# Performance work log

Hardware: AMD Instinct MI355X
Metric: run time of the kernel (lower is better)

## Reference

```python
import jax, jax.numpy as jnp
import numpy as np
from jax import lax

B = 16384
N_NUM = 32
N_CAT = 16
D = 256
D_HID = 512
N_LAYERS = 8
VOCAB = 100001  # total_cats + 1
OUT_DIM = 2
TOT_FEAT = N_NUM + N_CAT
EPS = 1e-5


def _layernorm(x, g, b):
    mu = jnp.mean(x, axis=-1, keepdims=True)
    var = jnp.mean(jnp.square(x - mu), axis=-1, keepdims=True)
    return (x - mu) * lax.rsqrt(var + EPS) * g + b


def setup_inputs() -> dict:
    key = jax.random.key(0)
    ks = jax.random.split(key, 16)
    s = 0.02
    return {
        "x_numerical": jax.random.normal(ks[0], (B, N_NUM, 1), dtype=jnp.float32),
        "x_categorical_idx": jax.random.randint(ks[1], (B, N_CAT), 0, VOCAB - 1, dtype=jnp.int32),
        # per-feature Linear(1, D): weight [N_NUM, D], bias [N_NUM, D]
        "w_num": jax.random.normal(ks[2], (N_NUM, D), dtype=jnp.float32) * s,
        "b_num": jnp.zeros((N_NUM, D), dtype=jnp.float32),
        "cat_embed": jax.random.normal(ks[3], (VOCAB, D), dtype=jnp.float32) * s,
        "W_first": jax.random.normal(ks[4], (TOT_FEAT * D, D), dtype=jnp.float32) * s,
        "b_first": jnp.zeros((D,), dtype=jnp.float32),
        # stacked block params, leading dim = N_LAYERS
        "ln_g": jnp.ones((N_LAYERS, D), dtype=jnp.float32),
        "ln_b": jnp.zeros((N_LAYERS, D), dtype=jnp.float32),
        "W1s": jax.random.normal(ks[5], (N_LAYERS, D, D_HID), dtype=jnp.float32) * s,
        "b1s": jnp.zeros((N_LAYERS, D_HID), dtype=jnp.float32),
        "W2s": jax.random.normal(ks[6], (N_LAYERS, D_HID, D), dtype=jnp.float32) * s,
        "b2s": jnp.zeros((N_LAYERS, D), dtype=jnp.float32),
        "g_f": jnp.ones((D,), dtype=jnp.float32),
        "beta_f": jnp.zeros((D,), dtype=jnp.float32),
        "W_head": jax.random.normal(ks[7], (D, OUT_DIM), dtype=jnp.float32) * s,
        "b_head": jnp.zeros((OUT_DIM,), dtype=jnp.float32),
    }


def reference(x_numerical, x_categorical_idx, w_num, b_num, cat_embed,
              W_first, b_first, ln_g, ln_b, W1s, b1s, W2s, b2s,
              g_f, beta_f, W_head, b_head):
    # numerical embeddings: per-feature Linear(1, D), vectorized over features
    x_val = x_numerical[:, :, 0:1]                       # [B, N_NUM, 1]
    x_n_emb = x_val * w_num[None] + b_num[None]          # [B, N_NUM, D]
    x_c_emb = cat_embed[x_categorical_idx]               # [B, N_CAT, D]
    x = jnp.concatenate([x_n_emb, x_c_emb], axis=1)      # [B, TOT_FEAT, D]
    x = x.reshape(x.shape[0], -1)                        # [B, TOT_FEAT*D]
    x = x @ W_first + b_first                            # [B, D]

    def block(h, params):
        g, bn, W1, b1, W2, b2 = params
        out = _layernorm(h, g, bn)
        out = jax.nn.relu(out @ W1 + b1)                 # dropout = identity (eval)
        out = out @ W2 + b2
        return h + out, None

    x, _ = lax.scan(block, x, (ln_g, ln_b, W1s, b1s, W2s, b2s))
    x = _layernorm(x, g_f, beta_f)
    logits = x @ W_head + b_head                         # [B, OUT_DIM]
    return logits
```

## Files before the change

kernel.cpp:

```cpp
#include <hip/hip_runtime.h>

typedef unsigned short u16;
typedef unsigned int u32;
typedef __attribute__((ext_vector_type(8))) short bf16x8;
typedef __attribute__((ext_vector_type(4))) float f32x4;

#define LDK 72

__device__ __forceinline__ u16 f2bf(float f) {
    u32 u = __float_as_uint(f);
    u += 0x7fffu + ((u >> 16) & 1u);
    return (u16)(u >> 16);
}

__device__ __forceinline__ f32x4 mfma16(bf16x8 a, bf16x8 b, f32x4 c) {
    return __builtin_amdgcn_mfma_f32_16x16x32_bf16(a, b, c, 0, 0, 0);
}


__global__ __launch_bounds__(256) void prep_u_kernel(
    const float* __restrict__ w_num, const float* __restrict__ b_num,
    const float* __restrict__ W_first, float* __restrict__ U, float* __restrict__ P)
{
    __shared__ float wrow[256];
    __shared__ float brow[256];
    int j = threadIdx.x, f = blockIdx.x;
    wrow[j] = w_num[f * 256 + j];
    brow[j] = b_num[f * 256 + j];
    __syncthreads();
    float au = 0.f, ap = 0.f;
#pragma unroll 8
    for (int k = 0; k < 256; k++) {
        float w = W_first[(size_t)((f << 8) + k) * 256 + j];
        au = fmaf(wrow[k], w, au);
        ap = fmaf(brow[k], w, ap);
    }
    U[f * 256 + j] = au;
    P[f * 256 + j] = ap;
}

__global__ __launch_bounds__(256) void prep_c0_kernel(
    const float* __restrict__ b_first, const float* __restrict__ P, float* __restrict__ c0)
{
    int j = threadIdx.x;
    float a = b_first[j];
#pragma unroll 8
    for (int f = 0; f < 32; f++) a += P[f * 256 + j];
    c0[j] = a;
}

__global__ __launch_bounds__(256) void transpose_kernel(
    const float* __restrict__ in, u16* __restrict__ out,
    int R, int C, int ldo, int k_off, size_t in_stride, size_t out_stride)
{
    __shared__ float t[64][65];
    in  += (size_t)blockIdx.z * in_stride;
    out += (size_t)blockIdx.z * out_stride;
    const int tid = threadIdx.x;
    const int r0 = blockIdx.x * 64, c0 = blockIdx.y * 64;
#pragma unroll
    for (int i = 0; i < 16; i++) {
        int e = tid + i * 256;
        int r = e >> 6, c = e & 63;
        float v = (r0 + r < R) ? in[(size_t)(r0 + r) * C + c0 + c] : 0.f;
        t[c][r] = v;
    }
    __syncthreads();
#pragma unroll
    for (int i = 0; i < 2; i++) {
        int e = tid + i * 256;
        int c = e >> 3, r8 = (e & 7) * 8;
        u16 tmp[8];
#pragma unroll
        for (int x = 0; x < 8; x++) tmp[x] = f2bf(t[c][r8 + x]);
        *(bf16x8*)&out[(size_t)(c0 + c) * ldo + k_off + r0 + r8] = *(bf16x8*)tmp;
    }
}

#define FBM 64

#define GATHER(KQ, G0, G1)                                                    \
    {                                                                         \
        int chunk = tid;                                                      \
        int r = chunk >> 4, c4 = chunk & 15;                                  \
        int k = (KQ) + c4 * 4;                                                \
        int rowi = (k < 4096) ? sidx[r * 16 + ((k >> 8) & 15)] : 0;           \
        G0 = *(const float4*)&cemb[(size_t)rowi * 256 + (k & 255)];           \
        if (k >= 4096) {                                                      \
            if (k < 4128) {                                                   \
                int c = r * 32 + (k - 4096);                                  \
                G0.x = sx[c]; G0.y = sx[c + 1];                               \
                G0.z = sx[c + 2]; G0.w = sx[c + 3];                           \
            } else G0 = make_float4(0.f, 0.f, 0.f, 0.f);                      \
        }                                                                     \
        chunk = tid + 512;                                                    \
        r = chunk >> 4; c4 = chunk & 15;                                      \
        k = (KQ) + c4 * 4;                                                    \
        rowi = (k < 4096) ? sidx[r * 16 + ((k >> 8) & 15)] : 0;               \
        G1 = *(const float4*)&cemb[(size_t)rowi * 256 + (k & 255)];           \
        if (k >= 4096) {                                                      \
            if (k < 4128) {                                                   \
                int c = r * 32 + (k - 4096);                                  \
                G1.x = sx[c]; G1.y = sx[c + 1];                               \
                G1.z = sx[c + 2]; G1.w = sx[c + 3];                           \
            } else G1 = make_float4(0.f, 0.f, 0.f, 0.f);                      \
        }                                                                     \
    }

#define WRITE_A(BUF, G0, G1)                                                  \
    {                                                                         \
        int chunk = tid;                                                      \
        int r = chunk >> 4, c4 = chunk & 15;                                  \
        ushort4 o;                                                            \
        o.x = f2bf(G0.x); o.y = f2bf(G0.y); o.z = f2bf(G0.z); o.w = f2bf(G0.w); \
        *(ushort4*)&Ab[BUF][r * LDK + c4 * 4] = o;                            \
        chunk = tid + 512;                                                    \
        r = chunk >> 4; c4 = chunk & 15;                                      \
        o.x = f2bf(G1.x); o.y = f2bf(G1.y); o.z = f2bf(G1.z); o.w = f2bf(G1.w); \
        *(ushort4*)&Ab[BUF][r * LDK + c4 * 4] = o;                            \
    }

#define DMA_B(BUF, KQ)                                                        \
    _Pragma("unroll")                                                         \
    for (int it = 0; it < 4; it++) {                                          \
        int chunk = it * 512 + tid;                                           \
        int r = chunk >> 3;                                                   \
        int c8 = (chunk & 7) ^ (r & 7);                                       \
        const u16* src = &BT[(size_t)r * 4160 + (KQ) + c8 * 8];               \
        __builtin_amdgcn_global_load_lds(                                     \
            (const __attribute__((address_space(1))) void*)src,               \
            (__attribute__((address_space(3))) void*)&Bb[BUF][(it * 512 + wv * 64) * 8], \
            16, 0, 0);                                                        \
    }

#define COMPUTE(CUR)                                                          \
    _Pragma("unroll")                                                         \
    for (int kk = 0; kk < 64; kk += 32) {                                     \
        bf16x8 af[2], bfr[4];                                                 \
        _Pragma("unroll")                                                     \
        for (int i = 0; i < 2; i++)                                           \
            af[i] = *(const bf16x8*)&Ab[CUR][(wm * 32 + i * 16 + l16) * LDK + kk + quad * 8]; \
        _Pragma("unroll")                                                     \
        for (int j = 0; j < 4; j++) {                                         \
            int row = wn * 64 + j * 16 + l16;                                 \
            int c8L = quad + (kk >> 3);                                       \
            bfr[j] = *(const bf16x8*)&Bb[CUR][row * 64 + ((c8L ^ (row & 7)) * 8)]; \
        }                                                                     \
        _Pragma("unroll")                                                     \
        for (int i = 0; i < 2; i++)                                           \
            _Pragma("unroll")                                                 \
            for (int j = 0; j < 4; j++)                                       \
                acc[i][j] = mfma16(af[i], bfr[j], acc[i][j]);                 \
    }

#define ITER_MAIN(CUR, KQ, GA0, GA1)                                          \
    {                                                                         \
        WRITE_A(CUR ^ 1, GA0, GA1);                                           \
        DMA_B(CUR ^ 1, (KQ) + 64);                                            \
        __builtin_amdgcn_sched_barrier(0);                                    \
        GATHER((KQ) + 192, GA0, GA1);                                         \
        COMPUTE(CUR);                                                         \
        asm volatile("s_waitcnt vmcnt(2) lgkmcnt(0)" ::: "memory");           \
        __builtin_amdgcn_s_barrier();                                         \
        __builtin_amdgcn_sched_barrier(0);                                    \
    }

__global__ __launch_bounds__(512, 2) void first_gemm_kernel(
    const u16* __restrict__ BT, const float* __restrict__ bias,
    float* __restrict__ outF,
    const int* __restrict__ cidx, const float* __restrict__ cemb,
    const float* __restrict__ xnum)
{
    __shared__ __align__(16) u16 Ab[2][FBM * LDK];
    __shared__ __align__(16) u16 Bb[2][256 * 64];
    __shared__ int   sidx[FBM * 16];
    __shared__ float sx[FBM * 32];

    const int tid  = threadIdx.x;
    const int lane = tid & 63;
    const int wv   = tid >> 6;
    const int wm   = wv >> 2;
    const int wn   = wv & 3;
    const int quad = lane >> 4;
    const int l16  = lane & 15;
    const int m0   = blockIdx.x * FBM;

    sidx[tid]       = cidx[m0 * 16 + tid];
    sidx[tid + 512] = cidx[m0 * 16 + tid + 512];
    {
        float4 v = *(const float4*)&xnum[(size_t)m0 * 32 + tid * 4];
        *(float4*)&sx[tid * 4] = v;
    }
    __syncthreads();

    f32x4 acc[2][4];
#pragma unroll
    for (int i = 0; i < 2; i++)
#pragma unroll
        for (int j = 0; j < 4; j++) acc[i][j] = (f32x4){0.f, 0.f, 0.f, 0.f};

    float4 pa0, pa1, pb0, pb1;

    GATHER(0, pa0, pa1);
    WRITE_A(0, pa0, pa1);
    DMA_B(0, 0);
    __builtin_amdgcn_sched_barrier(0);
    GATHER(64, pa0, pa1);
    GATHER(128, pb0, pb1);
    asm volatile("s_waitcnt vmcnt(4) lgkmcnt(0)" ::: "memory");
    __builtin_amdgcn_s_barrier();
    __builtin_amdgcn_sched_barrier(0);

#pragma unroll 1
    for (int k0 = 0; k0 < 4096; k0 += 128) {
        ITER_MAIN(0, k0,      pa0, pa1);
        ITER_MAIN(1, k0 + 64, pb0, pb1);
    }
    COMPUTE(0);

#pragma unroll
    for (int i = 0; i < 2; i++) {
#pragma unroll
        for (int j = 0; j < 4; j++) {
            int col = wn * 64 + j * 16 + l16;
            float bs = bias[col];
#pragma unroll
            for (int r = 0; r < 4; r++) {
                int row = m0 + wm * 32 + i * 16 + quad * 4 + r;
                outF[(size_t)row * 256 + col] = acc[i][j][r] + bs;
            }
        }
    }
}

__global__ __launch_bounds__(512, 2) void layer_kernel(
    float* __restrict__ h,
    const float* __restrict__ g, const float* __restrict__ bta,
    const u16* __restrict__ W1, const float* __restrict__ b1,
    const u16* __restrict__ W2, const float* __restrict__ b2)
{
    __shared__ __align__(16) u16 hn[64 * 264];
    __shared__ __align__(16) u16 hid[64 * 520];
    const int tid  = threadIdx.x;
    const int lane = tid & 63;
    const int wv   = tid >> 6;
    const int quad = lane >> 4;
    const int l16  = lane & 15;
    const int m0   = blockIdx.x * 64;

    float4 gv4 = *(const float4*)&g[lane * 4];
    float4 bv4 = *(const float4*)&bta[lane * 4];
#pragma unroll
    for (int rr = 0; rr < 8; rr++) {
        int row = rr * 8 + wv;
        float4 x = *(const float4*)&h[(size_t)(m0 + row) * 256 + lane * 4];
        float s  = x.x + x.y + x.z + x.w;
        float s2 = x.x * x.x + x.y * x.y + x.z * x.z + x.w * x.w;
#pragma unroll
        for (int o = 32; o > 0; o >>= 1) { s += __shfl_xor(s, o); s2 += __shfl_xor(s2, o); }
        float mu = s * (1.f / 256.f);
        float rs = rsqrtf(s2 * (1.f / 256.f) - mu * mu + 1e-5f);
        ushort4 o4;
        o4.x = f2bf((x.x - mu) * rs * gv4.x + bv4.x);
        o4.y = f2bf((x.y - mu) * rs * gv4.y + bv4.y);
        o4.z = f2bf((x.z - mu) * rs * gv4.z + bv4.z);
        o4.w = f2bf((x.w - mu) * rs * gv4.w + bv4.w);
        *(ushort4*)&hn[row * 264 + lane * 4] = o4;
    }
    __syncthreads();

    float b1v[4];
#pragma unroll
    for (int j = 0; j < 4; j++) b1v[j] = b1[wv * 64 + j * 16 + l16];
    f32x4 acc1[4][4];
#pragma unroll
    for (int i = 0; i < 4; i++)
#pragma unroll
        for (int j = 0; j < 4; j++) acc1[i][j] = (f32x4){0.f, 0.f, 0.f, 0.f};
#pragma unroll
    for (int kk = 0; kk < 256; kk += 32) {
        bf16x8 af[4], bw[4];
#pragma unroll
        for (int i = 0; i < 4; i++)
            af[i] = *(const bf16x8*)&hn[(i * 16 + l16) * 264 + kk + quad * 8];
#pragma unroll
        for (int j = 0; j < 4; j++)
            bw[j] = *(const bf16x8*)&W1[(size_t)(wv * 64 + j * 16 + l16) * 256 + kk + quad * 8];
#pragma unroll
        for (int i = 0; i < 4; i++)
#pragma unroll
            for (int j = 0; j < 4; j++)
                acc1[i][j] = mfma16(af[i], bw[j], acc1[i][j]);
    }
#pragma unroll
    for (int i = 0; i < 4; i++)
#pragma unroll
        for (int j = 0; j < 4; j++)
#pragma unroll
            for (int r = 0; r < 4; r++) {
                float v = acc1[i][j][r] + b1v[j];
                v = v > 0.f ? v : 0.f;
                hid[(i * 16 + quad * 4 + r) * 520 + wv * 64 + j * 16 + l16] = f2bf(v);
            }
    __syncthreads();

    float b2v[2];
#pragma unroll
    for (int j = 0; j < 2; j++) b2v[j] = b2[wv * 32 + j * 16 + l16];
    f32x4 acc2[4][2];
#pragma unroll
    for (int i = 0; i < 4; i++)
#pragma unroll
        for (int j = 0; j < 2; j++) acc2[i][j] = (f32x4){0.f, 0.f, 0.f, 0.f};
#pragma unroll
    for (int kk = 0; kk < 512; kk += 32) {
        bf16x8 af[4], bw[2];
#pragma unroll
        for (int i = 0; i < 4; i++)
            af[i] = *(const bf16x8*)&hid[(i * 16 + l16) * 520 + kk + quad * 8];
#pragma unroll
        for (int j = 0; j < 2; j++)
            bw[j] = *(const bf16x8*)&W2[(size_t)(wv * 32 + j * 16 + l16) * 512 + kk + quad * 8];
#pragma unroll
        for (int i = 0; i < 4; i++)
#pragma unroll
            for (int j = 0; j < 2; j++)
                acc2[i][j] = mfma16(af[i], bw[j], acc2[i][j]);
    }
    __syncthreads();

    float* hstore = (float*)hid;
#pragma unroll
    for (int i = 0; i < 4; i++)
#pragma unroll
        for (int j = 0; j < 2; j++) {
            int col = wv * 32 + j * 16 + l16;
#pragma unroll
            for (int r = 0; r < 4; r++)
                hstore[(i * 16 + quad * 4 + r) * 260 + col] = acc2[i][j][r] + b2v[j];
        }
    __syncthreads();
#pragma unroll
    for (int rr = 0; rr < 8; rr++) {
        int row = rr * 8 + wv;
        float4 v = *(const float4*)&hstore[row * 260 + lane * 4];
        float4 res = *(const float4*)&h[(size_t)(m0 + row) * 256 + lane * 4];
        v.x += res.x; v.y += res.y; v.z += res.z; v.w += res.w;
        *(float4*)&h[(size_t)(m0 + row) * 256 + lane * 4] = v;
    }
}

__global__ __launch_bounds__(256) void head_kernel(
    const float* __restrict__ h, const float* __restrict__ g,
    const float* __restrict__ bta, const float* __restrict__ Wh,
    const float* __restrict__ bh, float* __restrict__ out)
{
    int lane = threadIdx.x & 63;
    int row = blockIdx.x * 4 + (threadIdx.x >> 6);
    const float4 x = *(const float4*)&h[(size_t)row * 256 + lane * 4];
    float s = x.x + x.y + x.z + x.w;
    float s2 = x.x * x.x + x.y * x.y + x.z * x.z + x.w * x.w;
    for (int o = 32; o > 0; o >>= 1) { s += __shfl_xor(s, o); s2 += __shfl_xor(s2, o); }
    float mu = s * (1.f / 256.f);
    float rs = rsqrtf(s2 * (1.f / 256.f) - mu * mu + 1e-5f);
    float4 gv = *(const float4*)&g[lane * 4];
    float4 bv = *(const float4*)&bta[lane * 4];
    float xn0 = (x.x - mu) * rs * gv.x + bv.x;
    float xn1 = (x.y - mu) * rs * gv.y + bv.y;
    float xn2 = (x.z - mu) * rs * gv.z + bv.z;
    float xn3 = (x.w - mu) * rs * gv.w + bv.w;
    float4 wa = *(const float4*)&Wh[lane * 8];
    float4 wb = *(const float4*)&Wh[lane * 8 + 4];
    float d0 = xn0 * wa.x + xn1 * wa.z + xn2 * wb.x + xn3 * wb.z;
    float d1 = xn0 * wa.y + xn1 * wa.w + xn2 * wb.y + xn3 * wb.w;
    for (int o = 32; o > 0; o >>= 1) { d0 += __shfl_xor(d0, o); d1 += __shfl_xor(d1, o); }
    if (lane == 0) {
        out[(size_t)row * 2 + 0] = d0 + bh[0];
        out[(size_t)row * 2 + 1] = d1 + bh[1];
    }
}

extern "C" void kernel_launch(void* const* d_in, const int* in_sizes, int n_in,
                              void* d_out, int out_size, void* d_ws, size_t ws_size,
                              hipStream_t stream)
{
    const float* x_num   = (const float*)d_in[0];
    const int*   cidx    = (const int*)d_in[1];
    const float* w_num   = (const float*)d_in[2];
    const float* b_num   = (const float*)d_in[3];
    const float* cemb    = (const float*)d_in[4];
    const float* W_first = (const float*)d_in[5];
    const float* b_first = (const float*)d_in[6];
    const float* ln_g    = (const float*)d_in[7];
    const float* ln_b    = (const float*)d_in[8];
    const float* W1s     = (const float*)d_in[9];
    const float* b1s     = (const float*)d_in[10];
    const float* W2s     = (const float*)d_in[11];
    const float* b2s     = (const float*)d_in[12];
    const float* g_f     = (const float*)d_in[13];
    const float* beta_f  = (const float*)d_in[14];
    const float* W_head  = (const float*)d_in[15];
    const float* b_head  = (const float*)d_in[16];
    float* out = (float*)d_out;

    char* ws = (char*)d_ws;
    float* U   = (float*)(ws + 0);
    float* c0  = (float*)(ws + 32768);
    float* P   = (float*)(ws + 33792);
    u16* WcT   = (u16*)(ws + 66560);
    u16* W1T   = (u16*)(ws + 2196480);
    u16* W2T   = (u16*)(ws + 4293632);
    float* h   = (float*)(ws + 6390784);

    prep_u_kernel<<<32, 256, 0, stream>>>(w_num, b_num, W_first, U, P);
    prep_c0_kernel<<<1, 256, 0, stream>>>(b_first, P, c0);
    transpose_kernel<<<dim3(64, 4, 1), 256, 0, stream>>>(
        W_first + (size_t)8192 * 256, WcT, 4096, 256, 4160, 0, 0, 0);
    transpose_kernel<<<dim3(1, 4, 1), 256, 0, stream>>>(
        U, WcT, 32, 256, 4160, 4096, 0, 0);
    transpose_kernel<<<dim3(4, 8, 8), 256, 0, stream>>>(
        W1s, W1T, 256, 512, 256, 0, 131072, 131072);
    transpose_kernel<<<dim3(8, 4, 8), 256, 0, stream>>>(
        W2s, W2T, 512, 256, 512, 0, 131072, 131072);

    first_gemm_kernel<<<256, 512, 0, stream>>>(
        WcT, c0, h, cidx, cemb, x_num);

    for (int l = 0; l < 8; l++) {
        layer_kernel<<<256, 512, 0, stream>>>(
            h, ln_g + l * 256, ln_b + l * 256,
            W1T + (size_t)l * 131072, b1s + l * 512,
            W2T + (size_t)l * 131072, b2s + l * 256);
    }
    head_kernel<<<4096, 256, 0, stream>>>(h, g_f, beta_f, W_head, b_head, out);
}
```

Before: 497.6 us.

## Fuse all residual layers and head into one kernel; deepen B prefetch

Replaces the eight per-layer launches and the head kernel with a single stack_kernel that keeps each 64-row tile of h resident in LDS across all layers. It applies the residual adds in shared memory and finishes with the final layernorm and head. This removes repeated global round-trips of h and the per-launch overhead. Separately, the first GEMM gets a four-deep B buffer ring with prefetch distance two to hide DMA latency, which raises LDS use and may lower occupancy.

```diff
diff --git a/kernel.cpp b/kernel.cpp
--- a/kernel.cpp
+++ b/kernel.cpp
@@ -133,18 +133,18 @@
             16, 0, 0);                                                        \
     }
 
-#define COMPUTE(CUR)                                                          \
+#define COMPUTE(AB, BB)                                                       \
     _Pragma("unroll")                                                         \
     for (int kk = 0; kk < 64; kk += 32) {                                     \
         bf16x8 af[2], bfr[4];                                                 \
         _Pragma("unroll")                                                     \
         for (int i = 0; i < 2; i++)                                           \
-            af[i] = *(const bf16x8*)&Ab[CUR][(wm * 32 + i * 16 + l16) * LDK + kk + quad * 8]; \
+            af[i] = *(const bf16x8*)&Ab[AB][(wm * 32 + i * 16 + l16) * LDK + kk + quad * 8]; \
         _Pragma("unroll")                                                     \
         for (int j = 0; j < 4; j++) {                                         \
             int row = wn * 64 + j * 16 + l16;                                 \
             int c8L = quad + (kk >> 3);                                       \
-            bfr[j] = *(const bf16x8*)&Bb[CUR][row * 64 + ((c8L ^ (row & 7)) * 8)]; \
+            bfr[j] = *(const bf16x8*)&Bb[BB][row * 64 + ((c8L ^ (row & 7)) * 8)]; \
         }                                                                     \
         _Pragma("unroll")                                                     \
         for (int i = 0; i < 2; i++)                                           \
@@ -153,14 +153,16 @@
                 acc[i][j] = mfma16(af[i], bfr[j], acc[i][j]);                 \
     }
 
-#define ITER_MAIN(CUR, KQ, GA0, GA1)                                          \
+#define ITER(S, KQ, G0, G1)                                                   \
     {                                                                         \
-        WRITE_A(CUR ^ 1, GA0, GA1);                                           \
-        DMA_B(CUR ^ 1, (KQ) + 64);                                            \
+        WRITE_A((S + 1) & 1, G0, G1);                                         \
+        int kq2 = (KQ) + 128; if (kq2 > 4096) kq2 = 4096;                     \
+        DMA_B((S + 2) & 3, kq2);                                              \
         __builtin_amdgcn_sched_barrier(0);                                    \
-        GATHER((KQ) + 192, GA0, GA1);                                         \
-        COMPUTE(CUR);                                                         \
-        asm volatile("s_waitcnt vmcnt(2) lgkmcnt(0)" ::: "memory");           \
+        GATHER((KQ) + 192, G0, G1);                                           \
+        __builtin_amdgcn_sched_barrier(0);                                    \
+        COMPUTE(S & 1, S);                                                    \
+        asm volatile("s_waitcnt vmcnt(8) lgkmcnt(0)" ::: "memory");           \
         __builtin_amdgcn_s_barrier();                                         \
         __builtin_amdgcn_sched_barrier(0);                                    \
     }
@@ -172,7 +174,7 @@
     const float* __restrict__ xnum)
 {
     __shared__ __align__(16) u16 Ab[2][FBM * LDK];
-    __shared__ __align__(16) u16 Bb[2][256 * 64];
+    __shared__ __align__(16) u16 Bb[4][256 * 64];
     __shared__ int   sidx[FBM * 16];
     __shared__ float sx[FBM * 32];
 
@@ -199,24 +201,30 @@
 #pragma unroll
         for (int j = 0; j < 4; j++) acc[i][j] = (f32x4){0.f, 0.f, 0.f, 0.f};
 
-    float4 pa0, pa1, pb0, pb1;
-
-    GATHER(0, pa0, pa1);
-    WRITE_A(0, pa0, pa1);
+    float4 ga0, ga1, pa0, pa1, pb0, pb1;
+
+    GATHER(0, ga0, ga1);
+    WRITE_A(0, ga0, ga1);
     DMA_B(0, 0);
     __builtin_amdgcn_sched_barrier(0);
     GATHER(64, pa0, pa1);
+    __builtin_amdgcn_sched_barrier(0);
+    DMA_B(1, 64);
+    __builtin_amdgcn_sched_barrier(0);
     GATHER(128, pb0, pb1);
-    asm volatile("s_waitcnt vmcnt(4) lgkmcnt(0)" ::: "memory");
+    __builtin_amdgcn_sched_barrier(0);
+    asm volatile("s_waitcnt vmcnt(8) lgkmcnt(0)" ::: "memory");
     __builtin_amdgcn_s_barrier();
     __builtin_amdgcn_sched_barrier(0);
 
 #pragma unroll 1
-    for (int k0 = 0; k0 < 4096; k0 += 128) {
-        ITER_MAIN(0, k0,      pa0, pa1);
-        ITER_MAIN(1, k0 + 64, pb0, pb1);
-    }
-    COMPUTE(0);
+    for (int k0 = 0; k0 < 4096; k0 += 256) {
+        ITER(0, k0 +   0, pa0, pa1);
+        ITER(1, k0 +  64, pb0, pb1);
+        ITER(2, k0 + 128, pa0, pa1);
+        ITER(3, k0 + 192, pb0, pb1);
+    }
+    COMPUTE(0, 0);
 
 #pragma unroll
     for (int i = 0; i < 2; i++) {
@@ -233,14 +241,17 @@
     }
 }
 
-__global__ __launch_bounds__(512, 2) void layer_kernel(
-    float* __restrict__ h,
-    const float* __restrict__ g, const float* __restrict__ bta,
-    const u16* __restrict__ W1, const float* __restrict__ b1,
-    const u16* __restrict__ W2, const float* __restrict__ b2)
-{
-    __shared__ __align__(16) u16 hn[64 * 264];
-    __shared__ __align__(16) u16 hid[64 * 520];
+__global__ __launch_bounds__(512, 2) void stack_kernel(
+    const float* __restrict__ h,
+    const float* __restrict__ ln_g, const float* __restrict__ ln_b,
+    const u16* __restrict__ W1T, const float* __restrict__ b1s,
+    const u16* __restrict__ W2T, const float* __restrict__ b2s,
+    const float* __restrict__ g_f, const float* __restrict__ beta_f,
+    const float* __restrict__ Wh, const float* __restrict__ bh,
+    float* __restrict__ out)
+{
+    __shared__ __align__(16) float hbuf[64 * 260];
+    __shared__ __align__(16) u16   scratch[64 * 520];
     const int tid  = threadIdx.x;
     const int lane = tid & 63;
     const int wv   = tid >> 6;
@@ -248,135 +259,144 @@
     const int l16  = lane & 15;
     const int m0   = blockIdx.x * 64;
 
-    float4 gv4 = *(const float4*)&g[lane * 4];
-    float4 bv4 = *(const float4*)&bta[lane * 4];
 #pragma unroll
     for (int rr = 0; rr < 8; rr++) {
         int row = rr * 8 + wv;
-        float4 x = *(const float4*)&h[(size_t)(m0 + row) * 256 + lane * 4];
-        float s  = x.x + x.y + x.z + x.w;
-        float s2 = x.x * x.x + x.y * x.y + x.z * x.z + x.w * x.w;
-#pragma unroll
-        for (int o = 32; o > 0; o >>= 1) { s += __shfl_xor(s, o); s2 += __shfl_xor(s2, o); }
-        float mu = s * (1.f / 256.f);
-        float rs = rsqrtf(s2 * (1.f / 256.f) - mu * mu + 1e-5f);
-        ushort4 o4;
-        o4.x = f2bf((x.x - mu) * rs * gv4.x + bv4.x);
-        o4.y = f2bf((x.y - mu) * rs * gv4.y + bv4.y);
-        o4.z = f2bf((x.z - mu) * rs * gv4.z + bv4.z);
-        o4.w = f2bf((x.w - mu) * rs * gv4.w + bv4.w);
-        *(ushort4*)&hn[row * 264 + lane * 4] = o4;
+        *(float4*)&hbuf[row * 260 + lane * 4] =
+            *(const float4*)&h[(size_t)(m0 + row) * 256 + lane * 4];
     }
     __syncthreads();
 
-    float b1v[4];
-#pragma unroll
-    for (int j = 0; j < 4; j++) b1v[j] = b1[wv * 64 + j * 16 + l16];
-    f32x4 acc1[4][4];
-#pragma unroll
-    for (int i = 0; i < 4; i++)
-#pragma unroll
-        for (int j = 0; j < 4; j++) acc1[i][j] = (f32x4){0.f, 0.f, 0.f, 0.f};
-#pragma unroll
-    for (int kk = 0; kk < 256; kk += 32) {
-        bf16x8 af[4], bw[4];
+#pragma unroll 1
+    for (int l = 0; l < 8; l++) {
+        const u16* W1 = W1T + l * 131072;
+        const u16* W2 = W2T + l * 131072;
+        const float* bb1 = b1s + l * 512;
+        const float* bb2 = b2s + l * 256;
+
+        float4 gv4 = *(const float4*)&ln_g[l * 256 + lane * 4];
+        float4 bv4 = *(const float4*)&ln_b[l * 256 + lane * 4];
+#pragma unroll
+        for (int rr = 0; rr < 8; rr++) {
+            int row = rr * 8 + wv;
+            float4 x = *(const float4*)&hbuf[row * 260 + lane * 4];
+            float s  = x.x + x.y + x.z + x.w;
+            float s2 = x.x * x.x + x.y * x.y + x.z * x.z + x.w * x.w;
+#pragma unroll
+            for (int o = 32; o > 0; o >>= 1) { s += __shfl_xor(s, o); s2 += __shfl_xor(s2, o); }
+            float mu = s * (1.f / 256.f);
+            float rs = rsqrtf(s2 * (1.f / 256.f) - mu * mu + 1e-5f);
+            ushort4 o4;
+            o4.x = f2bf((x.x - mu) * rs * gv4.x + bv4.x);
+            o4.y = f2bf((x.y - mu) * rs * gv4.y + bv4.y);
+            o4.z = f2bf((x.z - mu) * rs * gv4.z + bv4.z);
+            o4.w = f2bf((x.w - mu) * rs * gv4.w + bv4.w);
+            *(ushort4*)&scratch[row * 264 + lane * 4] = o4;
+        }
+        __syncthreads();
+
+        float b1v[4];
+#pragma unroll
+        for (int j = 0; j < 4; j++) b1v[j] = bb1[wv * 64 + j * 16 + l16];
+        f32x4 acc1[4][4];
 #pragma unroll
         for (int i = 0; i < 4; i++)
-            af[i] = *(const bf16x8*)&hn[(i * 16 + l16) * 264 + kk + quad * 8];
-#pragma unroll
-        for (int j = 0; j < 4; j++)
-            bw[j] = *(const bf16x8*)&W1[(size_t)(wv * 64 + j * 16 + l16) * 256 + kk + quad * 8];
+#pragma unroll
+            for (int j = 0; j < 4; j++) acc1[i][j] = (f32x4){0.f, 0.f, 0.f, 0.f};
+#pragma unroll
+        for (int kk = 0; kk < 256; kk += 32) {
+            bf16x8 af[4], bw[4];
+#pragma unroll
+            for (int i = 0; i < 4; i++)
+                af[i] = *(const bf16x8*)&scratch[(i * 16 + l16) * 264 + kk + quad * 8];
+#pragma unroll
+            for (int j = 0; j < 4; j++)
+                bw[j] = *(const bf16x8*)&W1[(size_t)(wv * 64 + j * 16 + l16) * 256 + kk + quad * 8];
+#pragma unroll
+            for (int i = 0; i < 4; i++)
+#pragma unroll
+                for (int j = 0; j < 4; j++)
+                    acc1[i][j] = mfma16(af[i], bw[j], acc1[i][j]);
+        }
+        __syncthreads();
+
 #pragma unroll
         for (int i = 0; i < 4; i++)
 #pragma unroll
             for (int j = 0; j < 4; j++)
-                acc1[i][j] = mfma16(af[i], bw[j], acc1[i][j]);
-    }
-#pragma unroll
-    for (int i = 0; i < 4; i++)
-#pragma unroll
-        for (int j = 0; j < 4; j++)
-#pragma unroll
-            for (int r = 0; r < 4; r++) {
-                float v = acc1[i][j][r] + b1v[j];
-                v = v > 0.f ? v : 0.f;
-                hid[(i * 16 + quad * 4 + r) * 520 + wv * 64 + j * 16 + l16] = f2bf(v);
+#pragma unroll
+                for (int r = 0; r < 4; r++) {
+                    float v = acc1[i][j][r] + b1v[j];
+                    v = v > 0.f ? v : 0.f;
+                    scratch[(i * 16 + quad * 4 + r) * 520 + wv * 64 + j * 16 + l16] = f2bf(v);
+                }
+        __syncthreads();
+
+        float b2v[2];
+#pragma unroll
+        for (int j = 0; j < 2; j++) b2v[j] = bb2[wv * 32 + j * 16 + l16];
+        f32x4 acc2[4][2];
+#pragma unroll
+        for (int i = 0; i < 4; i++)
+#pragma unroll
+            for (int j = 0; j < 2; j++) acc2[i][j] = (f32x4){0.f, 0.f, 0.f, 0.f};
+#pragma unroll
+        for (int kk = 0; kk < 512; kk += 32) {
+            bf16x8 af[4], bw[2];
+#pragma unroll
+            for (int i = 0; i < 4; i++)
+                af[i] = *(const bf16x8*)&scratch[(i * 16 + l16) * 520 + kk + quad * 8];
+#pragma unroll
+            for (int j = 0; j < 2; j++)
+                bw[j] = *(const bf16x8*)&W2[(size_t)(wv * 32 + j * 16 + l16) * 512 + kk + quad * 8];
+#pragma unroll
+            for (int i = 0; i < 4; i++)
+#pragma unroll
+                for (int j = 0; j < 2; j++)
+                    acc2[i][j] = mfma16(af[i], bw[j], acc2[i][j]);
+        }
+
+#pragma unroll
+        for (int i = 0; i < 4; i++)
+#pragma unroll
+            for (int j = 0; j < 2; j++) {
+                int col = wv * 32 + j * 16 + l16;
+#pragma unroll
+                for (int r = 0; r < 4; r++)
+                    hbuf[(i * 16 + quad * 4 + r) * 260 + col] += acc2[i][j][r] + b2v[j];
             }
-    __syncthreads();
-
-    float b2v[2];
-#pragma unroll
-    for (int j = 0; j < 2; j++) b2v[j] = b2[wv * 32 + j * 16 + l16];
-    f32x4 acc2[4][2];
-#pragma unroll
-    for (int i = 0; i < 4; i++)
-#pragma unroll
-        for (int j = 0; j < 2; j++) acc2[i][j] = (f32x4){0.f, 0.f, 0.f, 0.f};
-#pragma unroll
-    for (int kk = 0; kk < 512; kk += 32) {
-        bf16x8 af[4], bw[2];
-#pragma unroll
-        for (int i = 0; i < 4; i++)
-            af[i] = *(const bf16x8*)&hid[(i * 16 + l16) * 520 + kk + quad * 8];
-#pragma unroll
-        for (int j = 0; j < 2; j++)
-            bw[j] = *(const bf16x8*)&W2[(size_t)(wv * 32 + j * 16 + l16) * 512 + kk + quad * 8];
-#pragma unroll
-        for (int i = 0; i < 4; i++)
-#pragma unroll
-            for (int j = 0; j < 2; j++)
-                acc2[i][j] = mfma16(af[i], bw[j], acc2[i][j]);
-    }
-    __syncthreads();
-
-    float* hstore = (float*)hid;
-#pragma unroll
-    for (int i = 0; i < 4; i++)
-#pragma unroll
-        for (int j = 0; j < 2; j++) {
-            int col = wv * 32 + j * 16 + l16;
-#pragma unroll
-            for (int r = 0; r < 4; r++)
-                hstore[(i * 16 + quad * 4 + r) * 260 + col] = acc2[i][j][r] + b2v[j];
+        __syncthreads();
+    }
+
+    {
+        float4 gv4 = *(const float4*)&g_f[lane * 4];
+        float4 bv4 = *(const float4*)&beta_f[lane * 4];
+        float4 wa = *(const float4*)&Wh[lane * 8];
+        float4 wb = *(const float4*)&Wh[lane * 8 + 4];
+        float bh0 = bh[0], bh1 = bh[1];
+#pragma unroll
+        for (int rr = 0; rr < 8; rr++) {
+            int row = rr * 8 + wv;
+            float4 x = *(const float4*)&hbuf[row * 260 + lane * 4];
+            float s = x.x + x.y + x.z + x.w;
+            float s2 = x.x * x.x + x.y * x.y + x.z * x.z + x.w * x.w;
+#pragma unroll
+            for (int o = 32; o > 0; o >>= 1) { s += __shfl_xor(s, o); s2 += __shfl_xor(s2, o); }
+            float mu = s * (1.f / 256.f);
+            float rs = rsqrtf(s2 * (1.f / 256.f) - mu * mu + 1e-5f);
+            float xn0 = (x.x - mu) * rs * gv4.x + bv4.x;
+            float xn1 = (x.y - mu) * rs * gv4.y + bv4.y;
+            float xn2 = (x.z - mu) * rs * gv4.z + bv4.z;
+            float xn3 = (x.w - mu) * rs * gv4.w + bv4.w;
+            float d0 = xn0 * wa.x + xn1 * wa.z + xn2 * wb.x + xn3 * wb.z;
+            float d1 = xn0 * wa.y + xn1 * wa.w + xn2 * wb.y + xn3 * wb.w;
+#pragma unroll
+            for (int o = 32; o > 0; o >>= 1) { d0 += __shfl_xor(d0, o); d1 += __shfl_xor(d1, o); }
+            if (lane == 0) {
+                out[(size_t)(m0 + row) * 2 + 0] = d0 + bh0;
+                out[(size_t)(m0 + row) * 2 + 1] = d1 + bh1;
+            }
         }
-    __syncthreads();
-#pragma unroll
-    for (int rr = 0; rr < 8; rr++) {
-        int row = rr * 8 + wv;
-        float4 v = *(const float4*)&hstore[row * 260 + lane * 4];
-        float4 res = *(const float4*)&h[(size_t)(m0 + row) * 256 + lane * 4];
-        v.x += res.x; v.y += res.y; v.z += res.z; v.w += res.w;
-        *(float4*)&h[(size_t)(m0 + row) * 256 + lane * 4] = v;
-    }
-}
-
-__global__ __launch_bounds__(256) void head_kernel(
-    const float* __restrict__ h, const float* __restrict__ g,
-    const float* __restrict__ bta, const float* __restrict__ Wh,
-    const float* __restrict__ bh, float* __restrict__ out)
-{
-    int lane = threadIdx.x & 63;
-    int row = blockIdx.x * 4 + (threadIdx.x >> 6);
-    const float4 x = *(const float4*)&h[(size_t)row * 256 + lane * 4];
-    float s = x.x + x.y + x.z + x.w;
-    float s2 = x.x * x.x + x.y * x.y + x.z * x.z + x.w * x.w;
-    for (int o = 32; o > 0; o >>= 1) { s += __shfl_xor(s, o); s2 += __shfl_xor(s2, o); }
-    float mu = s * (1.f / 256.f);
-    float rs = rsqrtf(s2 * (1.f / 256.f) - mu * mu + 1e-5f);
-    float4 gv = *(const float4*)&g[lane * 4];
-    float4 bv = *(const float4*)&bta[lane * 4];
-    float xn0 = (x.x - mu) * rs * gv.x + bv.x;
-    float xn1 = (x.y - mu) * rs * gv.y + bv.y;
-    float xn2 = (x.z - mu) * rs * gv.z + bv.z;
-    float xn3 = (x.w - mu) * rs * gv.w + bv.w;
-    float4 wa = *(const float4*)&Wh[lane * 8];
-    float4 wb = *(const float4*)&Wh[lane * 8 + 4];
-    float d0 = xn0 * wa.x + xn1 * wa.z + xn2 * wb.x + xn3 * wb.z;
-    float d1 = xn0 * wa.y + xn1 * wa.w + xn2 * wb.y + xn3 * wb.w;
-    for (int o = 32; o > 0; o >>= 1) { d0 += __shfl_xor(d0, o); d1 += __shfl_xor(d1, o); }
-    if (lane == 0) {
-        out[(size_t)row * 2 + 0] = d0 + bh[0];
-        out[(size_t)row * 2 + 1] = d1 + bh[1];
     }
 }
 
@@ -426,11 +446,7 @@
     first_gemm_kernel<<<256, 512, 0, stream>>>(
         WcT, c0, h, cidx, cemb, x_num);
 
-    for (int l = 0; l < 8; l++) {
-        layer_kernel<<<256, 512, 0, stream>>>(
-            h, ln_g + l * 256, ln_b + l * 256,
-            W1T + (size_t)l * 131072, b1s + l * 512,
-            W2T + (size_t)l * 131072, b2s + l * 256);
-    }
-    head_kernel<<<4096, 256, 0, stream>>>(h, g_f, beta_f, W_head, b_head, out);
-}
+    stack_kernel<<<256, 512, 0, stream>>>(
+        h, ln_g, ln_b, W1T, b1s, W2T, b2s,
+        g_f, beta_f, W_head, b_head, out);
+}
```

Result: faster. 458.4 us (-7.9%).
